# Kernel optimization log

Measured on AMD Instinct MI355X. Metric: run time of the kernel, lower is better.

Reference implementation:

```python
import jax, jax.numpy as jnp
import numpy as np

N, E = 50000, 800000
D_LLM, D_PLM, D_HID, N_CLS = 256, 256, 256, 40
BN_EPS = 1e-5


def _batchnorm(x, w, b):
    # training-mode BatchNorm1d: batch mean, biased variance
    m = x.mean(0)
    v = x.var(0)
    return (x - m) * jax.lax.rsqrt(v + BN_EPS) * w + b


def _sage_mean(feat, src, dst, w_self, w_neigh, b_neigh):
    # DGL SAGEConv('mean'): fc_self(h) + fc_neigh(mean over in-neighbors)
    n = feat.shape[0]
    ones = jnp.ones(src.shape[0], feat.dtype)
    deg = jax.ops.segment_sum(ones, dst, num_segments=n)            # in-degree
    agg = jax.ops.segment_sum(feat[src], dst, num_segments=n)      # [N, d]
    agg = agg / jnp.maximum(deg, 1.0)[:, None]                     # zero-deg -> 0
    return feat @ w_self.T + agg @ w_neigh.T + b_neigh


def setup_inputs() -> dict:
    key = jax.random.key(0)
    ks = jax.random.split(key, 16)
    w = lambda k, shape: jax.random.normal(k, shape, jnp.float32) * 0.05
    return {
        "LLM_feat": jax.random.normal(ks[0], (N, D_LLM), jnp.float32),
        "PLM_feat": jax.random.normal(ks[1], (N, D_PLM), jnp.float32),
        "src": jax.random.randint(ks[2], (E,), 0, N, jnp.int32),
        "dst": jax.random.randint(ks[3], (E,), 0, N, jnp.int32),
        "w_self_0": w(ks[4], (D_PLM, D_LLM)),
        "w_neigh_0": w(ks[5], (D_PLM, D_LLM)),
        "b_neigh_0": jnp.zeros((D_PLM,), jnp.float32),
        "w_self_1": w(ks[6], (D_HID, D_PLM)),
        "w_neigh_1": w(ks[7], (D_HID, D_PLM)),
        "b_neigh_1": jnp.zeros((D_HID,), jnp.float32),
        "w_self_2": w(ks[8], (N_CLS, D_HID)),
        "w_neigh_2": w(ks[9], (N_CLS, D_HID)),
        "b_neigh_2": jnp.zeros((N_CLS,), jnp.float32),
        "bn0_w": jnp.ones((D_PLM,), jnp.float32),
        "bn0_b": jnp.zeros((D_PLM,), jnp.float32),
        "bn1_w": jnp.ones((D_HID,), jnp.float32),
        "bn1_b": jnp.zeros((D_HID,), jnp.float32),
    }


def reference(LLM_feat, PLM_feat, src, dst,
              w_self_0, w_neigh_0, b_neigh_0,
              w_self_1, w_neigh_1, b_neigh_1,
              w_self_2, w_neigh_2, b_neigh_2,
              bn0_w, bn0_b, bn1_w, bn1_b):
    # layer 0: SAGE -> BN, residual add of BN(PLM_feat) (same norm module), relu
    h = _sage_mean(LLM_feat, src, dst, w_self_0, w_neigh_0, b_neigh_0)
    h = _batchnorm(h, bn0_w, bn0_b) + _batchnorm(PLM_feat, bn0_w, bn0_b)
    h = jax.nn.relu(h)  # dropout p=0.0 -> identity
    # layer 1
    h = _sage_mean(h, src, dst, w_self_1, w_neigh_1, b_neigh_1)
    h = jax.nn.relu(_batchnorm(h, bn1_w, bn1_b))
    # layer 2 (output, no norm/activation)
    h = _sage_mean(h, src, dst, w_self_2, w_neigh_2, b_neigh_2)
    return h
```

## Files before the change

### kernel.cpp

```cpp
#include <hip/hip_runtime.h>

#define N_NODES 50000
#define N_EDGES 800000
#define D 256
#define NCLS 40
#define NP 50176
#define NB 196
#define BN_EPS 1e-5f

typedef __attribute__((ext_vector_type(8))) short bf16x8;
typedef __attribute__((ext_vector_type(4))) float f32x4;

__device__ __forceinline__ unsigned short f2bf(float x) {
  unsigned u = __builtin_bit_cast(unsigned, x);
  unsigned r = (u + 0x7FFFu + ((u >> 16) & 1u)) >> 16;
  return (unsigned short)r;
}
__device__ __forceinline__ float bf2f(unsigned short h) {
  unsigned u = ((unsigned)h) << 16;
  return __builtin_bit_cast(float, u);
}

__global__ void k_hist(const int* __restrict__ dst, int* __restrict__ cnt) {
  int i = blockIdx.x * blockDim.x + threadIdx.x;
  int stride = gridDim.x * blockDim.x;
  for (; i < N_EDGES; i += stride) atomicAdd(&cnt[dst[i] + 1], 1);
}

__global__ void k_scan1(int* __restrict__ a, int* __restrict__ bsum) {
  __shared__ int s[256];
  int i = blockIdx.x * 256 + threadIdx.x;
  s[threadIdx.x] = a[i];
  __syncthreads();
#pragma unroll
  for (int o = 1; o < 256; o <<= 1) {
    int t = (threadIdx.x >= o) ? s[threadIdx.x - o] : 0;
    __syncthreads();
    s[threadIdx.x] += t;
    __syncthreads();
  }
  a[i] = s[threadIdx.x];
  if (threadIdx.x == 255) bsum[blockIdx.x] = s[255];
}

__global__ void k_scan2(int* __restrict__ bsum) {
  __shared__ int s[256];
  int t = threadIdx.x;
  s[t] = (t < NB) ? bsum[t] : 0;
  __syncthreads();
#pragma unroll
  for (int o = 1; o < 256; o <<= 1) {
    int x = (t >= o) ? s[t - o] : 0;
    __syncthreads();
    s[t] += x;
    __syncthreads();
  }
  if (t < NB) bsum[t] = (t == 0) ? 0 : s[t - 1];
}

__global__ void k_scan3(int* __restrict__ a, const int* __restrict__ bsum) {
  if (blockIdx.x == 0) return;
  int i = blockIdx.x * 256 + threadIdx.x;
  a[i] += bsum[blockIdx.x];
}

__global__ void k_copycur(const int* __restrict__ off, int* __restrict__ cur) {
  int i = blockIdx.x * blockDim.x + threadIdx.x;
  if (i < N_NODES) cur[i] = off[i];
}

__global__ void k_fill(const int* __restrict__ src, const int* __restrict__ dst,
                       int* __restrict__ cur, int* __restrict__ esrc) {
  int i = blockIdx.x * blockDim.x + threadIdx.x;
  int stride = gridDim.x * blockDim.x;
  for (; i < N_EDGES; i += stride) {
    int p = atomicAdd(&cur[dst[i]], 1);
    esrc[p] = src[i];
  }
}

__global__ __launch_bounds__(256) void k_gather_bf(const unsigned short* __restrict__ feat,
                                                   const int* __restrict__ off,
                                                   const int* __restrict__ esrc,
                                                   unsigned short* __restrict__ aggout) {
  int wave = blockIdx.x * 4 + (threadIdx.x >> 6);
  int lane = threadIdx.x & 63;
  if (wave >= N_NODES) return;
  int s0 = off[wave], s1 = off[wave + 1];
  float a0 = 0.f, a1 = 0.f, a2 = 0.f, a3 = 0.f;
  int j = s0;
  for (; j + 3 < s1; j += 4) {
    int sa = esrc[j], sb = esrc[j + 1], sc = esrc[j + 2], sd = esrc[j + 3];
    ushort4 va = *(const ushort4*)&feat[(size_t)sa * 512 + lane * 4];
    ushort4 vb = *(const ushort4*)&feat[(size_t)sb * 512 + lane * 4];
    ushort4 vc = *(const ushort4*)&feat[(size_t)sc * 512 + lane * 4];
    ushort4 vd = *(const ushort4*)&feat[(size_t)sd * 512 + lane * 4];
    a0 += (bf2f(va.x) + bf2f(vb.x)) + (bf2f(vc.x) + bf2f(vd.x));
    a1 += (bf2f(va.y) + bf2f(vb.y)) + (bf2f(vc.y) + bf2f(vd.y));
    a2 += (bf2f(va.z) + bf2f(vb.z)) + (bf2f(vc.z) + bf2f(vd.z));
    a3 += (bf2f(va.w) + bf2f(vb.w)) + (bf2f(vc.w) + bf2f(vd.w));
  }
  for (; j < s1; ++j) {
    int sa = esrc[j];
    ushort4 va = *(const ushort4*)&feat[(size_t)sa * 512 + lane * 4];
    a0 += bf2f(va.x); a1 += bf2f(va.y); a2 += bf2f(va.z); a3 += bf2f(va.w);
  }
  float inv = 1.0f / fmaxf((float)(s1 - s0), 1.0f);
  ushort4 o;
  o.x = f2bf(a0 * inv); o.y = f2bf(a1 * inv);
  o.z = f2bf(a2 * inv); o.w = f2bf(a3 * inv);
  *(ushort4*)&aggout[(size_t)wave * 512 + lane * 4] = o;
}

__global__ __launch_bounds__(256) void k_gather40(const float* __restrict__ P,
                                                  const int* __restrict__ off,
                                                  const int* __restrict__ esrc,
                                                  const float* __restrict__ b2,
                                                  float* __restrict__ out) {
  int wave = blockIdx.x * 4 + (threadIdx.x >> 6);
  int lane = threadIdx.x & 63;
  if (wave >= N_NODES || lane >= NCLS) return;
  int s0 = off[wave], s1 = off[wave + 1];
  float acc = 0.f;
  int j = s0;
  for (; j + 3 < s1; j += 4) {
    int sa = esrc[j], sb = esrc[j + 1], sc = esrc[j + 2], sd = esrc[j + 3];
    float va = P[(size_t)sa * 80 + NCLS + lane];
    float vb = P[(size_t)sb * 80 + NCLS + lane];
    float vc = P[(size_t)sc * 80 + NCLS + lane];
    float vd = P[(size_t)sd * 80 + NCLS + lane];
    acc += (va + vb) + (vc + vd);
  }
  for (; j < s1; ++j) {
    int s = esrc[j];
    acc += P[(size_t)s * 80 + NCLS + lane];
  }
  float inv = 1.0f / fmaxf((float)(s1 - s0), 1.0f);
  out[(size_t)wave * NCLS + lane] = P[(size_t)wave * 80 + lane] + b2[lane] + acc * inv;
}

__global__ void k_cvt(const float* __restrict__ x, unsigned short* __restrict__ hi,
                      unsigned short* __restrict__ lo) {
  int i = blockIdx.x * blockDim.x + threadIdx.x;
  int stride = gridDim.x * blockDim.x;
  const int n4 = N_NODES * D / 4;
  for (; i < n4; i += stride) {
    int row = i >> 6;
    int c4 = (i & 63) * 4;
    float4 v = ((const float4*)x)[i];
    ushort4 h, l;
    h.x = f2bf(v.x); l.x = f2bf(v.x - bf2f(h.x));
    h.y = f2bf(v.y); l.y = f2bf(v.y - bf2f(h.y));
    h.z = f2bf(v.z); l.z = f2bf(v.z - bf2f(h.z));
    h.w = f2bf(v.w); l.w = f2bf(v.w - bf2f(h.w));
    *(ushort4*)&hi[(size_t)row * 512 + c4] = h;
    *(ushort4*)&lo[(size_t)row * 256 + c4] = l;
  }
}

__global__ void k_wsplit512(const float* __restrict__ W1, const float* __restrict__ W2,
                            unsigned short* __restrict__ Wh, unsigned short* __restrict__ Wl) {
  int i = blockIdx.x * blockDim.x + threadIdx.x;
  if (i >= 256 * 128) return;
  int row = i >> 7;
  int c4 = (i & 127) * 4;
  const float* srcp = (c4 < 256) ? &W1[(size_t)row * 256 + c4] : &W2[(size_t)row * 256 + c4 - 256];
  float4 v = *(const float4*)srcp;
  ushort4 h, l;
  h.x = f2bf(v.x); l.x = f2bf(v.x - bf2f(h.x));
  h.y = f2bf(v.y); l.y = f2bf(v.y - bf2f(h.y));
  h.z = f2bf(v.z); l.z = f2bf(v.z - bf2f(h.z));
  h.w = f2bf(v.w); l.w = f2bf(v.w - bf2f(h.w));
  *(ushort4*)&Wh[(size_t)row * 512 + c4] = h;
  *(ushort4*)&Wl[(size_t)row * 512 + c4] = l;
}

__global__ void k_wsplit2(const float* __restrict__ ws2, const float* __restrict__ wn2,
                          unsigned short* __restrict__ Wh, unsigned short* __restrict__ Wl) {
  int i = blockIdx.x * blockDim.x + threadIdx.x;
  if (i >= 80 * 64) return;
  int row = i >> 6;
  int c4 = (i & 63) * 4;
  const float* srcp = (row < NCLS) ? &ws2[(size_t)row * 256 + c4]
                                   : &wn2[(size_t)(row - NCLS) * 256 + c4];
  float4 v = *(const float4*)srcp;
  ushort4 h, l;
  h.x = f2bf(v.x); l.x = f2bf(v.x - bf2f(h.x));
  h.y = f2bf(v.y); l.y = f2bf(v.y - bf2f(h.y));
  h.z = f2bf(v.z); l.z = f2bf(v.z - bf2f(h.z));
  h.w = f2bf(v.w); l.w = f2bf(v.w - bf2f(h.w));
  *(ushort4*)&Wh[(size_t)row * 256 + c4] = h;
  *(ushort4*)&Wl[(size_t)row * 256 + c4] = l;
}

template <int NSTEPS, int NLO, bool HASBIAS>
__global__ __launch_bounds__(256) void k_bgemm(
    const unsigned short* __restrict__ Ah, int strideA,
    const unsigned short* __restrict__ Al,
    const unsigned short* __restrict__ Wh, const unsigned short* __restrict__ Wl, int strideW,
    const float* __restrict__ bias,
    float* __restrict__ Out, int M, int ncol, int ldc) {
  __shared__ short sAh[128 * 64], sAl[128 * 64], sWh[128 * 64], sWl[128 * 64];
  const int tid = threadIdx.x;
  const int lane = tid & 63;
  const int wv = tid >> 6;
  const int wr = wv >> 1, wc = wv & 1;
  const int m0 = blockIdx.x * 128, n0 = blockIdx.y * 128;

  f32x4 acc[4][4] = {};

  const int sr = tid >> 1;
  const int sk2 = (tid & 1) * 32;

  int arow = m0 + sr; if (arow > M - 1) arow = M - 1;
  int wrow = n0 + sr; if (wrow > ncol - 1) wrow = ncol - 1;

#pragma unroll
  for (int s = 0; s < NSTEPS; ++s) {
    const bool withLo = (s < NLO);
    const int k0 = s * 64;
    const unsigned short* pa  = Ah + (size_t)arow * strideA + k0 + sk2;
    const unsigned short* pal = Al + (size_t)arow * 256 + k0 + sk2;
    const unsigned short* pw  = Wh + (size_t)wrow * strideW + k0 + sk2;
    const unsigned short* pwl = Wl + (size_t)wrow * strideW + k0 + sk2;
    bf16x8 ra[4], ral[4], rw[4], rwl[4];
#pragma unroll
    for (int c = 0; c < 4; ++c) {
      ra[c]  = *(const bf16x8*)(pa + c * 8);
      rw[c]  = *(const bf16x8*)(pw + c * 8);
      rwl[c] = *(const bf16x8*)(pwl + c * 8);
      if (withLo) ral[c] = *(const bf16x8*)(pal + c * 8);
    }
    __syncthreads();
#pragma unroll
    for (int c = 0; c < 4; ++c) {
      int byte = (sk2 + c * 8) * 2;
      int idx = (sr * 128 + (byte ^ ((sr & 7) << 4))) >> 1;
      *(bf16x8*)&sAh[idx] = ra[c];
      *(bf16x8*)&sWh[idx] = rw[c];
      *(bf16x8*)&sWl[idx] = rwl[c];
      if (withLo) *(bf16x8*)&sAl[idx] = ral[c];
    }
    __syncthreads();
#pragma unroll
    for (int ks = 0; ks < 2; ++ks) {
      bf16x8 a_h[4], a_l[4], w_h[4], w_l[4];
      const int kb = ks * 64 + (lane >> 4) * 16;
#pragma unroll
      for (int i = 0; i < 4; ++i) {
        int rowA = wr * 64 + i * 16 + (lane & 15);
        int adA = (rowA * 128 + (kb ^ ((rowA & 7) << 4))) >> 1;
        a_h[i] = *(bf16x8*)&sAh[adA];
        if (withLo) a_l[i] = *(bf16x8*)&sAl[adA];
        int rowW = wc * 64 + i * 16 + (lane & 15);
        int adW = (rowW * 128 + (kb ^ ((rowW & 7) << 4))) >> 1;
        w_h[i] = *(bf16x8*)&sWh[adW];
        w_l[i] = *(bf16x8*)&sWl[adW];
      }
#pragma unroll
      for (int i = 0; i < 4; ++i)
#pragma unroll
        for (int j = 0; j < 4; ++j) {
          acc[i][j] = __builtin_amdgcn_mfma_f32_16x16x32_bf16(a_h[i], w_h[j], acc[i][j], 0, 0, 0);
          acc[i][j] = __builtin_amdgcn_mfma_f32_16x16x32_bf16(a_h[i], w_l[j], acc[i][j], 0, 0, 0);
          if (withLo)
            acc[i][j] = __builtin_amdgcn_mfma_f32_16x16x32_bf16(a_l[i], w_h[j], acc[i][j], 0, 0, 0);
        }
    }
  }
#pragma unroll
  for (int j = 0; j < 4; ++j) {
    int col = n0 + wc * 64 + j * 16 + (lane & 15);
    if (col >= ncol) continue;
    float bv = HASBIAS ? bias[col] : 0.f;
#pragma unroll
    for (int i = 0; i < 4; ++i) {
#pragma unroll
      for (int r = 0; r < 4; ++r) {
        int row = m0 + wr * 64 + i * 16 + (lane >> 4) * 4 + r;
        if (row < M) Out[(size_t)row * ldc + col] = acc[i][j][r] + bv;
      }
    }
  }
}

__global__ void k_stats(const float* __restrict__ x, float* __restrict__ stats) {
  int c = threadIdx.x;
  float s = 0.f, ss = 0.f;
  for (int r = blockIdx.x; r < N_NODES; r += gridDim.x) {
    float v = x[(size_t)r * D + c];
    s += v; ss += v * v;
  }
  atomicAdd(&stats[c], s);
  atomicAdd(&stats[D + c], ss);
}

__global__ void k_bnparams(const float* __restrict__ stats, const float* __restrict__ w,
                           const float* __restrict__ b, float* __restrict__ bnp) {
  int set = blockIdx.x, c = threadIdx.x;
  const float* st = stats + (size_t)set * 2 * D;
  float m = st[c] * (1.0f / N_NODES);
  float var = st[D + c] * (1.0f / N_NODES) - m * m;
  float sc = rsqrtf(var + BN_EPS) * w[c];
  bnp[(size_t)set * 2 * D + c] = sc;
  bnp[(size_t)set * 2 * D + D + c] = b[c] - m * sc;
}

template <bool ADD2>
__global__ void k_fusebf(const float* __restrict__ h, const float* __restrict__ x2,
                         const float* __restrict__ bnp,
                         unsigned short* __restrict__ hi, unsigned short* __restrict__ lo) {
  int i = blockIdx.x * blockDim.x + threadIdx.x;
  int stride = gridDim.x * blockDim.x;
  const int n4 = N_NODES * D / 4;
  for (; i < n4; i += stride) {
    int row = i >> 6;
    int c4 = (i & 63) * 4;
    float4 hv = ((const float4*)h)[i];
    float4 sc = *(const float4*)&bnp[c4];
    float4 sh = *(const float4*)&bnp[D + c4];
    float4 o;
    o.x = hv.x * sc.x + sh.x; o.y = hv.y * sc.y + sh.y;
    o.z = hv.z * sc.z + sh.z; o.w = hv.w * sc.w + sh.w;
    if (ADD2) {
      float4 pv = ((const float4*)x2)[i];
      float4 sc2 = *(const float4*)&bnp[2 * D + c4];
      float4 sh2 = *(const float4*)&bnp[3 * D + c4];
      o.x += pv.x * sc2.x + sh2.x; o.y += pv.y * sc2.y + sh2.y;
      o.z += pv.z * sc2.z + sh2.z; o.w += pv.w * sc2.w + sh2.w;
    }
    o.x = fmaxf(o.x, 0.f); o.y = fmaxf(o.y, 0.f);
    o.z = fmaxf(o.z, 0.f); o.w = fmaxf(o.w, 0.f);
    ushort4 H, L;
    H.x = f2bf(o.x); L.x = f2bf(o.x - bf2f(H.x));
    H.y = f2bf(o.y); L.y = f2bf(o.y - bf2f(H.y));
    H.z = f2bf(o.z); L.z = f2bf(o.z - bf2f(H.z));
    H.w = f2bf(o.w); L.w = f2bf(o.w - bf2f(H.w));
    *(ushort4*)&hi[(size_t)row * 512 + c4] = H;
    *(ushort4*)&lo[(size_t)row * 256 + c4] = L;
  }
}

extern "C" void kernel_launch(void* const* d_in, const int* in_sizes, int n_in,
                              void* d_out, int out_size, void* d_ws, size_t ws_size,
                              hipStream_t stream) {
  const float* LLM = (const float*)d_in[0];
  const float* PLM = (const float*)d_in[1];
  const int* src = (const int*)d_in[2];
  const int* dst = (const int*)d_in[3];
  const float* ws0 = (const float*)d_in[4];
  const float* wn0 = (const float*)d_in[5];
  const float* b0  = (const float*)d_in[6];
  const float* ws1 = (const float*)d_in[7];
  const float* wn1 = (const float*)d_in[8];
  const float* b1  = (const float*)d_in[9];
  const float* ws2 = (const float*)d_in[10];
  const float* wn2 = (const float*)d_in[11];
  const float* b2  = (const float*)d_in[12];
  const float* bn0w = (const float*)d_in[13];
  const float* bn0b = (const float*)d_in[14];
  const float* bn1w = (const float*)d_in[15];
  const float* bn1b = (const float*)d_in[16];

  float* W = (float*)d_ws;
  float* f_out = W;
  float* f_P   = W + 8000000;
  unsigned short* u_hi = (unsigned short*)(W + 12800000);
  unsigned short* u_lo = (unsigned short*)(W + 25600000);
  int* i_off  = (int*)(W + 32000000);
  int* i_bsum = i_off + NP;
  int* i_cur  = i_bsum + 256;
  int* i_esrc = i_cur + 50048;
  unsigned short* u_w0h = (unsigned short*)(W + 33000000);
  unsigned short* u_w0l = u_w0h + 131072;
  unsigned short* u_w1h = u_w0l + 131072;
  unsigned short* u_w1l = u_w1h + 131072;
  unsigned short* u_w2h = u_w1l + 131072;
  unsigned short* u_w2l = u_w2h + 20480;
  float* f_stats = (float*)(u_w2l + 20480);
  float* f_bnp   = f_stats + 1024;

  hipMemsetAsync(i_off, 0, NP * sizeof(int), stream);
  hipMemsetAsync(f_stats, 0, 1024 * sizeof(float), stream);
  k_hist<<<2048, 256, 0, stream>>>(dst, i_off);
  k_scan1<<<NB, 256, 0, stream>>>(i_off, i_bsum);
  k_scan2<<<1, 256, 0, stream>>>(i_bsum);
  k_scan3<<<NB, 256, 0, stream>>>(i_off, i_bsum);
  k_copycur<<<(N_NODES + 255) / 256, 256, 0, stream>>>(i_off, i_cur);
  k_fill<<<2048, 256, 0, stream>>>(src, dst, i_cur, i_esrc);

  k_wsplit512<<<128, 256, 0, stream>>>(ws0, wn0, u_w0h, u_w0l);
  k_wsplit512<<<128, 256, 0, stream>>>(ws1, wn1, u_w1h, u_w1l);
  k_wsplit2<<<20, 256, 0, stream>>>(ws2, wn2, u_w2h, u_w2l);

  k_cvt<<<2048, 256, 0, stream>>>(LLM, u_hi, u_lo);
  k_gather_bf<<<12500, 256, 0, stream>>>(u_hi, i_off, i_esrc, u_hi + 256);
  k_bgemm<8, 4, true><<<dim3(391, 2), 256, 0, stream>>>(
      u_hi, 512, u_lo, u_w0h, u_w0l, 512, b0, f_out, N_NODES, 256, 256);
  k_stats<<<512, 256, 0, stream>>>(f_out, f_stats);
  k_stats<<<512, 256, 0, stream>>>(PLM, f_stats + 512);
  k_bnparams<<<2, 256, 0, stream>>>(f_stats, bn0w, bn0b, f_bnp);
  k_fusebf<true><<<2048, 256, 0, stream>>>(f_out, PLM, f_bnp, u_hi, u_lo);

  hipMemsetAsync(f_stats, 0, 512 * sizeof(float), stream);
  k_gather_bf<<<12500, 256, 0, stream>>>(u_hi, i_off, i_esrc, u_hi + 256);
  k_bgemm<8, 4, true><<<dim3(391, 2), 256, 0, stream>>>(
      u_hi, 512, u_lo, u_w1h, u_w1l, 512, b1, f_out, N_NODES, 256, 256);
  k_stats<<<512, 256, 0, stream>>>(f_out, f_stats);
  k_bnparams<<<1, 256, 0, stream>>>(f_stats, bn1w, bn1b, f_bnp);
  k_fusebf<false><<<2048, 256, 0, stream>>>(f_out, nullptr, f_bnp, u_hi, u_lo);

  k_bgemm<4, 4, false><<<dim3(391, 1), 256, 0, stream>>>(
      u_hi, 512, u_lo, u_w2h, u_w2l, 256, nullptr, f_P, N_NODES, 80, 80);
  k_gather40<<<12500, 256, 0, stream>>>(f_P, i_off, i_esrc, b2, (float*)d_out);
}
```

Baseline: 723.6 us.

## Read weight fragments directly from global memory and prefetch next A tile

After: 791.1 us. 1.09x slower.

```diff
diff --git a/kernel.cpp b/kernel.cpp
--- a/kernel.cpp
+++ b/kernel.cpp
@@ -200,7 +200,7 @@
     const unsigned short* __restrict__ Wh, const unsigned short* __restrict__ Wl, int strideW,
     const float* __restrict__ bias,
     float* __restrict__ Out, int M, int ncol, int ldc) {
-  __shared__ short sAh[128 * 64], sAl[128 * 64], sWh[128 * 64], sWl[128 * 64];
+  __shared__ short sAh[128 * 64], sAl[128 * 64];
   const int tid = threadIdx.x;
   const int lane = tid & 63;
   const int wv = tid >> 6;
@@ -211,51 +211,63 @@
 
   const int sr = tid >> 1;
   const int sk2 = (tid & 1) * 32;
-
   int arow = m0 + sr; if (arow > M - 1) arow = M - 1;
-  int wrow = n0 + sr; if (wrow > ncol - 1) wrow = ncol - 1;
+
+  int wrow[4];
+#pragma unroll
+  for (int i = 0; i < 4; ++i) {
+    int r = n0 + wc * 64 + i * 16 + (lane & 15);
+    wrow[i] = (r > ncol - 1) ? (ncol - 1) : r;
+  }
+  const int kfrag = (lane >> 4) * 8;
+
+  bf16x8 cA[4], cAl[4];
+  {
+    const unsigned short* pa  = Ah + (size_t)arow * strideA + sk2;
+    const unsigned short* pal = Al + (size_t)arow * 256 + sk2;
+#pragma unroll
+    for (int c = 0; c < 4; ++c) {
+      cA[c] = *(const bf16x8*)(pa + c * 8);
+      if (NLO > 0) cAl[c] = *(const bf16x8*)(pal + c * 8);
+    }
+  }
 
 #pragma unroll
   for (int s = 0; s < NSTEPS; ++s) {
     const bool withLo = (s < NLO);
     const int k0 = s * 64;
-    const unsigned short* pa  = Ah + (size_t)arow * strideA + k0 + sk2;
-    const unsigned short* pal = Al + (size_t)arow * 256 + k0 + sk2;
-    const unsigned short* pw  = Wh + (size_t)wrow * strideW + k0 + sk2;
-    const unsigned short* pwl = Wl + (size_t)wrow * strideW + k0 + sk2;
-    bf16x8 ra[4], ral[4], rw[4], rwl[4];
-#pragma unroll
-    for (int c = 0; c < 4; ++c) {
-      ra[c]  = *(const bf16x8*)(pa + c * 8);
-      rw[c]  = *(const bf16x8*)(pw + c * 8);
-      rwl[c] = *(const bf16x8*)(pwl + c * 8);
-      if (withLo) ral[c] = *(const bf16x8*)(pal + c * 8);
-    }
     __syncthreads();
 #pragma unroll
     for (int c = 0; c < 4; ++c) {
       int byte = (sk2 + c * 8) * 2;
       int idx = (sr * 128 + (byte ^ ((sr & 7) << 4))) >> 1;
-      *(bf16x8*)&sAh[idx] = ra[c];
-      *(bf16x8*)&sWh[idx] = rw[c];
-      *(bf16x8*)&sWl[idx] = rwl[c];
-      if (withLo) *(bf16x8*)&sAl[idx] = ral[c];
+      *(bf16x8*)&sAh[idx] = cA[c];
+      if (withLo) *(bf16x8*)&sAl[idx] = cAl[c];
+    }
+    if (s + 1 < NSTEPS) {
+      const int k1 = (s + 1) * 64;
+      const unsigned short* pa  = Ah + (size_t)arow * strideA + k1 + sk2;
+      const unsigned short* pal = Al + (size_t)arow * 256 + k1 + sk2;
+#pragma unroll
+      for (int c = 0; c < 4; ++c) {
+        cA[c] = *(const bf16x8*)(pa + c * 8);
+        if (s + 1 < NLO) cAl[c] = *(const bf16x8*)(pal + c * 8);
+      }
     }
     __syncthreads();
 #pragma unroll
     for (int ks = 0; ks < 2; ++ks) {
+      const int kb = ks * 64 + (lane >> 4) * 16;
       bf16x8 a_h[4], a_l[4], w_h[4], w_l[4];
-      const int kb = ks * 64 + (lane >> 4) * 16;
 #pragma unroll
       for (int i = 0; i < 4; ++i) {
         int rowA = wr * 64 + i * 16 + (lane & 15);
         int adA = (rowA * 128 + (kb ^ ((rowA & 7) << 4))) >> 1;
         a_h[i] = *(bf16x8*)&sAh[adA];
         if (withLo) a_l[i] = *(bf16x8*)&sAl[adA];
-        int rowW = wc * 64 + i * 16 + (lane & 15);
-        int adW = (rowW * 128 + (kb ^ ((rowW & 7) << 4))) >> 1;
-        w_h[i] = *(bf16x8*)&sWh[adW];
-        w_l[i] = *(bf16x8*)&sWl[adW];
+        const size_t woff = (size_t)wrow[i] * strideW + k0 + ks * 32 + kfrag;
+        w_h[i] = *(const bf16x8*)(Wh + woff);
+        w_l[i] = *(const bf16x8*)(Wl + woff);
       }
 #pragma unroll
       for (int i = 0; i < 4; ++i)
```

## Fuse BatchNorm statistics into GEMM epilogue and prefetch next K tile into registers

Applied to the files above, without the earlier changes.

Result: faster. 677.0 us (-6.4%).

```diff
diff --git a/kernel.cpp b/kernel.cpp
--- a/kernel.cpp
+++ b/kernel.cpp
@@ -193,13 +193,13 @@
   *(ushort4*)&Wl[(size_t)row * 256 + c4] = l;
 }
 
-template <int NSTEPS, int NLO, bool HASBIAS>
+template <int NSTEPS, int NLO, bool HASBIAS, bool STATS>
 __global__ __launch_bounds__(256) void k_bgemm(
     const unsigned short* __restrict__ Ah, int strideA,
     const unsigned short* __restrict__ Al,
     const unsigned short* __restrict__ Wh, const unsigned short* __restrict__ Wl, int strideW,
     const float* __restrict__ bias,
-    float* __restrict__ Out, int M, int ncol, int ldc) {
+    float* __restrict__ Out, int M, int ncol, int ldc, float* __restrict__ stats) {
   __shared__ short sAh[128 * 64], sAl[128 * 64], sWh[128 * 64], sWl[128 * 64];
   const int tid = threadIdx.x;
   const int lane = tid & 63;
@@ -211,26 +211,27 @@
 
   const int sr = tid >> 1;
   const int sk2 = (tid & 1) * 32;
-
   int arow = m0 + sr; if (arow > M - 1) arow = M - 1;
   int wrow = n0 + sr; if (wrow > ncol - 1) wrow = ncol - 1;
 
-#pragma unroll
-  for (int s = 0; s < NSTEPS; ++s) {
-    const bool withLo = (s < NLO);
-    const int k0 = s * 64;
-    const unsigned short* pa  = Ah + (size_t)arow * strideA + k0 + sk2;
-    const unsigned short* pal = Al + (size_t)arow * 256 + k0 + sk2;
-    const unsigned short* pw  = Wh + (size_t)wrow * strideW + k0 + sk2;
-    const unsigned short* pwl = Wl + (size_t)wrow * strideW + k0 + sk2;
-    bf16x8 ra[4], ral[4], rw[4], rwl[4];
+  bf16x8 ra[4], ral[4], rw[4], rwl[4];
+  {
+    const unsigned short* pa  = Ah + (size_t)arow * strideA + sk2;
+    const unsigned short* pal = Al + (size_t)arow * 256 + sk2;
+    const unsigned short* pw  = Wh + (size_t)wrow * strideW + sk2;
+    const unsigned short* pwl = Wl + (size_t)wrow * strideW + sk2;
 #pragma unroll
     for (int c = 0; c < 4; ++c) {
       ra[c]  = *(const bf16x8*)(pa + c * 8);
       rw[c]  = *(const bf16x8*)(pw + c * 8);
       rwl[c] = *(const bf16x8*)(pwl + c * 8);
-      if (withLo) ral[c] = *(const bf16x8*)(pal + c * 8);
-    }
+      if (NLO > 0) ral[c] = *(const bf16x8*)(pal + c * 8);
+    }
+  }
+
+#pragma unroll
+  for (int s = 0; s < NSTEPS; ++s) {
+    const bool withLo = (s < NLO);
     __syncthreads();
 #pragma unroll
     for (int c = 0; c < 4; ++c) {
@@ -240,6 +241,20 @@
       *(bf16x8*)&sWh[idx] = rw[c];
       *(bf16x8*)&sWl[idx] = rwl[c];
       if (withLo) *(bf16x8*)&sAl[idx] = ral[c];
+    }
+    if (s + 1 < NSTEPS) {
+      const int k1 = (s + 1) * 64;
+      const unsigned short* pa  = Ah + (size_t)arow * strideA + k1 + sk2;
+      const unsigned short* pal = Al + (size_t)arow * 256 + k1 + sk2;
+      const unsigned short* pw  = Wh + (size_t)wrow * strideW + k1 + sk2;
+      const unsigned short* pwl = Wl + (size_t)wrow * strideW + k1 + sk2;
+#pragma unroll
+      for (int c = 0; c < 4; ++c) {
+        ra[c]  = *(const bf16x8*)(pa + c * 8);
+        rw[c]  = *(const bf16x8*)(pw + c * 8);
+        rwl[c] = *(const bf16x8*)(pwl + c * 8);
+        if (s + 1 < NLO) ral[c] = *(const bf16x8*)(pal + c * 8);
+      }
     }
     __syncthreads();
 #pragma unroll
@@ -273,12 +288,25 @@
     int col = n0 + wc * 64 + j * 16 + (lane & 15);
     if (col >= ncol) continue;
     float bv = HASBIAS ? bias[col] : 0.f;
+    float s = 0.f, ss = 0.f;
 #pragma unroll
     for (int i = 0; i < 4; ++i) {
 #pragma unroll
       for (int r = 0; r < 4; ++r) {
         int row = m0 + wr * 64 + i * 16 + (lane >> 4) * 4 + r;
-        if (row < M) Out[(size_t)row * ldc + col] = acc[i][j][r] + bv;
+        if (row < M) {
+          float v = acc[i][j][r] + bv;
+          Out[(size_t)row * ldc + col] = v;
+          if (STATS) { s += v; ss += v * v; }
+        }
+      }
+    }
+    if (STATS) {
+      s  += __shfl_xor(s, 16);  s  += __shfl_xor(s, 32);
+      ss += __shfl_xor(ss, 16); ss += __shfl_xor(ss, 32);
+      if ((lane >> 4) == 0) {
+        atomicAdd(&stats[col], s);
+        atomicAdd(&stats[D + col], ss);
       }
     }
   }
@@ -395,22 +423,20 @@
 
   k_cvt<<<2048, 256, 0, stream>>>(LLM, u_hi, u_lo);
   k_gather_bf<<<12500, 256, 0, stream>>>(u_hi, i_off, i_esrc, u_hi + 256);
-  k_bgemm<8, 4, true><<<dim3(391, 2), 256, 0, stream>>>(
-      u_hi, 512, u_lo, u_w0h, u_w0l, 512, b0, f_out, N_NODES, 256, 256);
-  k_stats<<<512, 256, 0, stream>>>(f_out, f_stats);
+  k_bgemm<8, 4, true, true><<<dim3(391, 2), 256, 0, stream>>>(
+      u_hi, 512, u_lo, u_w0h, u_w0l, 512, b0, f_out, N_NODES, 256, 256, f_stats);
   k_stats<<<512, 256, 0, stream>>>(PLM, f_stats + 512);
   k_bnparams<<<2, 256, 0, stream>>>(f_stats, bn0w, bn0b, f_bnp);
   k_fusebf<true><<<2048, 256, 0, stream>>>(f_out, PLM, f_bnp, u_hi, u_lo);
 
   hipMemsetAsync(f_stats, 0, 512 * sizeof(float), stream);
   k_gather_bf<<<12500, 256, 0, stream>>>(u_hi, i_off, i_esrc, u_hi + 256);
-  k_bgemm<8, 4, true><<<dim3(391, 2), 256, 0, stream>>>(
-      u_hi, 512, u_lo, u_w1h, u_w1l, 512, b1, f_out, N_NODES, 256, 256);
-  k_stats<<<512, 256, 0, stream>>>(f_out, f_stats);
+  k_bgemm<8, 4, true, true><<<dim3(391, 2), 256, 0, stream>>>(
+      u_hi, 512, u_lo, u_w1h, u_w1l, 512, b1, f_out, N_NODES, 256, 256, f_stats);
   k_bnparams<<<1, 256, 0, stream>>>(f_stats, bn1w, bn1b, f_bnp);
   k_fusebf<false><<<2048, 256, 0, stream>>>(f_out, nullptr, f_bnp, u_hi, u_lo);
 
-  k_bgemm<4, 4, false><<<dim3(391, 1), 256, 0, stream>>>(
-      u_hi, 512, u_lo, u_w2h, u_w2l, 256, nullptr, f_P, N_NODES, 80, 80);
+  k_bgemm<4, 4, false, false><<<dim3(391, 1), 256, 0, stream>>>(
+      u_hi, 512, u_lo, u_w2h, u_w2l, 256, nullptr, f_P, N_NODES, 80, 80, nullptr);
   k_gather40<<<12500, 256, 0, stream>>>(f_P, i_off, i_esrc, b2, (float*)d_out);
 }
```
